# Performance work log

Hardware: AMD Instinct MI355X
Metric: run time of the kernel (lower is better)

Reference implementation:

```python
import jax, jax.numpy as jnp
import numpy as np

BASIS = 30
HIDDEN = 15
MAX_ATOMS = 30
NUM_ATOMS = 110
NUM_GAUSS = 56
T = 3
B = 2048


def setup_inputs() -> dict:
    key = jax.random.key(0)
    ks = jax.random.split(key, 16)
    Z = jax.random.randint(ks[0], (B, MAX_ATOMS), 0, NUM_ATOMS + 1)
    D = jax.random.uniform(ks[1], (B, MAX_ATOMS, MAX_ATOMS, NUM_GAUSS), dtype=jnp.float32)
    sizes = jax.random.randint(ks[2], (B,), 1, MAX_ATOMS + 1)
    s = 0.1
    C_embed = jax.random.normal(ks[3], (NUM_ATOMS + 1, BASIS), dtype=jnp.float32) * s
    df_w = jax.random.normal(ks[4], (NUM_GAUSS, BASIS), dtype=jnp.float32) * s
    df_b = jax.random.normal(ks[5], (BASIS,), dtype=jnp.float32) * s
    cf_w = jax.random.normal(ks[6], (BASIS, BASIS), dtype=jnp.float32) * s
    cf_b = jax.random.normal(ks[7], (BASIS,), dtype=jnp.float32) * s
    fc_w = jax.random.normal(ks[8], (BASIS, BASIS), dtype=jnp.float32) * s  # no bias
    mlp_w1 = jax.random.normal(ks[9], (BASIS, HIDDEN), dtype=jnp.float32) * s
    mlp_b1 = jax.random.normal(ks[10], (HIDDEN,), dtype=jnp.float32) * s
    mlp_w2 = jax.random.normal(ks[11], (HIDDEN, 1), dtype=jnp.float32) * s
    mlp_b2 = jax.random.normal(ks[12], (1,), dtype=jnp.float32) * s
    return {"Z": Z, "D": D, "sizes": sizes, "C_embed": C_embed, "df_w": df_w,
            "df_b": df_b, "cf_w": cf_w, "cf_b": cf_b, "fc_w": fc_w,
            "mlp_w1": mlp_w1, "mlp_b1": mlp_b1, "mlp_w2": mlp_w2, "mlp_b2": mlp_b2}


def reference(Z, D, sizes, C_embed, df_w, df_b, cf_w, cf_b, fc_w,
              mlp_w1, mlp_b1, mlp_w2, mlp_b2):
    # masks from sizes (mask_1d / mask_2d over max_atoms)
    ar = jnp.arange(MAX_ATOMS)
    m1 = (ar[None, :] < sizes[:, None]).astype(D.dtype)            # [B, A]
    m2 = m1[:, :, None] * m1[:, None, :]                           # [B, A, A]

    C = C_embed[Z]                                                 # [B, A, basis]
    d_hat = jnp.einsum('bijg,gk->bijk', D, df_w) + df_b            # [B, A, A, basis]

    for _ in range(T):
        X = C @ cf_w + cf_b                                        # [B, A, basis]
        X = X[:, :, None, :] * d_hat                               # [B, A, A, basis]
        X = jnp.tanh(jnp.einsum('bijh,hk->bijk', X, fc_w))         # [B, A, A, basis]
        C = C + (m2[..., None] * X).sum(axis=1)                    # sum over first atom axis

    E = jnp.tanh(C @ mlp_w1 + mlp_b1) @ mlp_w2 + mlp_b2            # [B, A, 1]
    E = E[..., 0]                                                  # [B, A]
    return (m1 * E).sum(axis=-1)                                   # [B]
```

## Files before the change

kernel.cpp:

```cpp
#include <hip/hip_runtime.h>
#include <hip/hip_bf16.h>

typedef __attribute__((ext_vector_type(8))) short bh8;
typedef __attribute__((ext_vector_type(4))) float f4;

#define MFMA_BF16 __builtin_amdgcn_mfma_f32_16x16x32_bf16

__device__ __forceinline__ unsigned cvtpk(float a, float b) {
  unsigned r;
  asm("v_cvt_pk_bf16_f32 %0, %1, %2" : "=v"(r) : "v"(a), "v"(b));
  return r;
}
__device__ __forceinline__ bh8 mk_bh8(unsigned a, unsigned b, unsigned c, unsigned d) {
  uint4 u;
  u.x = a; u.y = b; u.z = c; u.w = d;
  return __builtin_bit_cast(bh8, u);
}

__device__ __forceinline__ float fast_tanh(float x) {
  float e = __builtin_amdgcn_exp2f(x * 2.885390081777927f);
  return fmaf(-2.f, __builtin_amdgcn_rcpf(e + 1.f), 1.f);
}

__device__ __forceinline__ short bf16hi(float f, float* hf) {
  __hip_bfloat16 h = __float2bfloat16(f);
  *hf = __bfloat162float(h);
  short s;
  __builtin_memcpy(&s, &h, 2);
  return s;
}
__device__ __forceinline__ short bf16s(float f) {
  __hip_bfloat16 h = __float2bfloat16(f);
  short s;
  __builtin_memcpy(&s, &h, 2);
  return s;
}


__global__ __launch_bounds__(256, 4) void mdtnn_phA_mfma(
    const float* __restrict__ Dg, const int* __restrict__ sizesg,
    const float* __restrict__ dfwg, const float* __restrict__ dfbg,
    uint2* __restrict__ dhg)
{
  const int b = blockIdx.x, tid = threadIdx.x;
  const int w = tid >> 6, l = tid & 63;
  const int lr = l & 15, lc = l >> 4;
  const int n = sizesg[b];
  const int nn = n * n;
  const unsigned inv = (65536u + (unsigned)n - 1) / (unsigned)n;

  bh8 Ah[2][2], Al[2][2];
  #pragma unroll
  for (int ht = 0; ht < 2; ++ht) {
    const int h = ht * 16 + lr;
    #pragma unroll
    for (int kc = 0; kc < 2; ++kc) {
      #pragma unroll
      for (int e = 0; e < 8; ++e) {
        const int g = kc * 32 + lc * 8 + e;
        float v = (g < 56 && h < 30) ? dfwg[g * 30 + h] : 0.f;
        float hf;
        Ah[ht][kc][e] = bf16hi(v, &hf);
        Al[ht][kc][e] = bf16s(v - hf);
      }
    }
  }
  float dfbv[2][4];
  #pragma unroll
  for (int ht = 0; ht < 2; ++ht)
    #pragma unroll
    for (int e = 0; e < 4; ++e) {
      const int h = ht * 16 + lc * 4 + e;
      dfbv[ht][e] = (h < 30) ? dfbg[h] : 0.f;
    }

  const float* Db = Dg + (size_t)b * (30 * 30 * 56);
  uint2* dhb = dhg + (size_t)b * (30 * 30 * 8);
  const f4 z4 = {0.f, 0.f, 0.f, 0.f};

  const int tiles = (nn + 15) >> 4;
  for (int t = w; t < tiles; t += 4) {
    const int p_raw = t * 16 + lr;
    const int p = min(p_raw, nn - 1);
    const int i = (int)(((unsigned)p * inv) >> 16);
    const int j = p - i * n;
    const int row = i * 30 + j;
    const float* Dp = Db + (size_t)row * 56;

    float4 q0 = *reinterpret_cast<const float4*>(Dp + lc * 8);
    float4 q1 = *reinterpret_cast<const float4*>(Dp + lc * 8 + 4);
    float4 q2 = {0.f, 0.f, 0.f, 0.f}, q3 = {0.f, 0.f, 0.f, 0.f};
    if (lc < 3) {
      q2 = *reinterpret_cast<const float4*>(Dp + 32 + lc * 8);
      q3 = *reinterpret_cast<const float4*>(Dp + 32 + lc * 8 + 4);
    }
    bh8 B0 = mk_bh8(cvtpk(q0.x, q0.y), cvtpk(q0.z, q0.w),
                    cvtpk(q1.x, q1.y), cvtpk(q1.z, q1.w));
    bh8 B1 = mk_bh8(cvtpk(q2.x, q2.y), cvtpk(q2.z, q2.w),
                    cvtpk(q3.x, q3.y), cvtpk(q3.z, q3.w));

    f4 a0 = z4, a1 = z4;
    a0 = MFMA_BF16(Al[0][0], B0, a0, 0, 0, 0);
    a0 = MFMA_BF16(Ah[0][0], B0, a0, 0, 0, 0);
    a0 = MFMA_BF16(Al[0][1], B1, a0, 0, 0, 0);
    a0 = MFMA_BF16(Ah[0][1], B1, a0, 0, 0, 0);
    a1 = MFMA_BF16(Al[1][0], B0, a1, 0, 0, 0);
    a1 = MFMA_BF16(Ah[1][0], B0, a1, 0, 0, 0);
    a1 = MFMA_BF16(Al[1][1], B1, a1, 0, 0, 0);
    a1 = MFMA_BF16(Ah[1][1], B1, a1, 0, 0, 0);

    if (p_raw < nn) {
      uint2 s0, s1;
      s0.x = cvtpk(a0[0] + dfbv[0][0], a0[1] + dfbv[0][1]);
      s0.y = cvtpk(a0[2] + dfbv[0][2], a0[3] + dfbv[0][3]);
      s1.x = cvtpk(a1[0] + dfbv[1][0], a1[1] + dfbv[1][1]);
      s1.y = cvtpk(a1[2] + dfbv[1][2], a1[3] + dfbv[1][3]);
      dhb[row * 8 + 0 * 4 + lc] = s0;
      dhb[row * 8 + 1 * 4 + lc] = s1;
    }
  }
}

__global__ __launch_bounds__(128, 3) void mdtnn_phB5(
    const int* __restrict__ Zg, const int* __restrict__ sizesg,
    const float* __restrict__ embg, const float* __restrict__ cfwg,
    const float* __restrict__ cfbg, const float* __restrict__ fcwg,
    const float* __restrict__ w1g, const float* __restrict__ b1g,
    const float* __restrict__ w2g, const float* __restrict__ b2g,
    const unsigned* __restrict__ dhg, float* __restrict__ outg)
{
  const int tid = threadIdx.x;
  const int wid = tid >> 6, l = tid & 63;
  const int lr = l & 15, lc = l >> 4;
  const int bm = blockIdx.x;

  __shared__ __align__(16) float buf[2][32][36];
  __shared__ __align__(16) float w1_s[32][16];
  __shared__ float b1_s[16], w2_s[16], wsum[2];

  for (int t = tid; t < 512; t += 128) {
    int k = t >> 4, c = t & 15;
    w1_s[k][c] = (k < 30 && c < 15) ? w1g[k * 15 + c] : 0.f;
  }
  if (tid < 16) {
    b1_s[tid] = (tid < 15) ? b1g[tid] : 0.f;
    w2_s[tid] = (tid < 15) ? w2g[tid] : 0.f;
  }

  const int n = sizesg[bm];
  float (*mybuf)[36] = buf[wid];

  float fcwF0[8], fcwF1[8];
  bh8 cfwB0h, cfwB0l, cfwB1h, cfwB1l;
  #pragma unroll
  for (int e = 0; e < 8; ++e) {
    const int kk = lc * 8 + e;
    const int c1 = lr + 16;
    fcwF0[e] = (kk < 30) ? fcwg[kk * 30 + lr] : 0.f;
    fcwF1[e] = (kk < 30 && c1 < 30) ? fcwg[kk * 30 + c1] : 0.f;
    float g0 = (kk < 30) ? cfwg[kk * 30 + lr] : 0.f;
    float g1 = (kk < 30 && c1 < 30) ? cfwg[kk * 30 + c1] : 0.f;
    float hf;
    cfwB0h[e] = bf16hi(g0, &hf);
    cfwB0l[e] = bf16s(g0 - hf);
    cfwB1h[e] = bf16hi(g1, &hf);
    cfwB1l[e] = bf16s(g1 - hf);
  }
  const float cfb0 = cfbg[lr];
  const float cfb1 = (lr + 16 < 30) ? cfbg[lr + 16] : 0.f;

  f4 C00, C01, C10, C11;
  #pragma unroll
  for (int e = 0; e < 4; ++e) {
    const int r0 = lc * 4 + e;
    const int r1 = 16 + lc * 4 + e;
    const int z0 = Zg[bm * 30 + r0];
    C00[e] = embg[z0 * 30 + lr];
    C01[e] = (lr + 16 < 30) ? embg[z0 * 30 + lr + 16] : 0.f;
    if (r1 < 30) {
      const int z1 = Zg[bm * 30 + r1];
      C10[e] = embg[z1 * 30 + lr];
      C11[e] = (lr + 16 < 30) ? embg[z1 * 30 + lr + 16] : 0.f;
    } else {
      C10[e] = 0.f;
      C11[e] = 0.f;
    }
  }

  const unsigned* dhb = dhg + (size_t)bm * 14400;
  const int n0 = (n + 1) >> 1;
  const int ibeg = wid ? n0 : 0;
  const int iend = wid ? n : n0;
  const f4 z4 = {0.f, 0.f, 0.f, 0.f};

  __syncthreads();

  for (int it = 0; it < 3; ++it) {
    uint4 a0c = {0, 0, 0, 0}, a1c = {0, 0, 0, 0};
    if (ibeg < iend) {
      const unsigned* p = dhb + (size_t)ibeg * 480;
      if (lr < n)      a0c = *reinterpret_cast<const uint4*>(p + lr * 16 + lc * 4);
      if (lr + 16 < n) a1c = *reinterpret_cast<const uint4*>(p + lr * 16 + 256 + lc * 4);
    }

    #pragma unroll
    for (int e = 0; e < 4; ++e) {
      mybuf[lc * 4 + e][lr]           = C00[e];
      mybuf[lc * 4 + e][lr + 16]      = C01[e];
      mybuf[16 + lc * 4 + e][lr]      = C10[e];
      mybuf[16 + lc * 4 + e][lr + 16] = C11[e];
    }
    float cv0[8], cv1[8];
    *reinterpret_cast<float4*>(&cv0[0]) = *reinterpret_cast<const float4*>(&mybuf[lr][lc * 8]);
    *reinterpret_cast<float4*>(&cv0[4]) = *reinterpret_cast<const float4*>(&mybuf[lr][lc * 8 + 4]);
    *reinterpret_cast<float4*>(&cv1[0]) = *reinterpret_cast<const float4*>(&mybuf[16 + lr][lc * 8]);
    *reinterpret_cast<float4*>(&cv1[4]) = *reinterpret_cast<const float4*>(&mybuf[16 + lr][lc * 8 + 4]);

    unsigned h_[4], lo_[4];
    #pragma unroll
    for (int q = 0; q < 4; ++q) {
      unsigned hq = cvtpk(cv0[2 * q], cv0[2 * q + 1]);
      float f0 = __uint_as_float(hq << 16);
      float f1 = __uint_as_float(hq & 0xffff0000u);
      h_[q] = hq;
      lo_[q] = cvtpk(cv0[2 * q] - f0, cv0[2 * q + 1] - f1);
    }
    bh8 Ch0 = mk_bh8(h_[0], h_[1], h_[2], h_[3]);
    bh8 Cl0 = mk_bh8(lo_[0], lo_[1], lo_[2], lo_[3]);
    #pragma unroll
    for (int q = 0; q < 4; ++q) {
      unsigned hq = cvtpk(cv1[2 * q], cv1[2 * q + 1]);
      float f0 = __uint_as_float(hq << 16);
      float f1 = __uint_as_float(hq & 0xffff0000u);
      h_[q] = hq;
      lo_[q] = cvtpk(cv1[2 * q] - f0, cv1[2 * q + 1] - f1);
    }
    bh8 Ch1 = mk_bh8(h_[0], h_[1], h_[2], h_[3]);
    bh8 Cl1 = mk_bh8(lo_[0], lo_[1], lo_[2], lo_[3]);

    f4 d00 = MFMA_BF16(Ch0, cfwB0l, z4, 0, 0, 0);
    d00 = MFMA_BF16(Cl0, cfwB0h, d00, 0, 0, 0);
    d00 = MFMA_BF16(Ch0, cfwB0h, d00, 0, 0, 0);
    f4 d01 = MFMA_BF16(Ch0, cfwB1l, z4, 0, 0, 0);
    d01 = MFMA_BF16(Cl0, cfwB1h, d01, 0, 0, 0);
    d01 = MFMA_BF16(Ch0, cfwB1h, d01, 0, 0, 0);
    f4 d10 = MFMA_BF16(Ch1, cfwB0l, z4, 0, 0, 0);
    d10 = MFMA_BF16(Cl1, cfwB0h, d10, 0, 0, 0);
    d10 = MFMA_BF16(Ch1, cfwB0h, d10, 0, 0, 0);
    f4 d11 = MFMA_BF16(Ch1, cfwB1l, z4, 0, 0, 0);
    d11 = MFMA_BF16(Cl1, cfwB1h, d11, 0, 0, 0);
    d11 = MFMA_BF16(Ch1, cfwB1h, d11, 0, 0, 0);
    #pragma unroll
    for (int e = 0; e < 4; ++e) {
      mybuf[lc * 4 + e][lr]           = d00[e] + cfb0;
      mybuf[lc * 4 + e][lr + 16]      = d01[e] + cfb1;
      mybuf[16 + lc * 4 + e][lr]      = d10[e] + cfb0;
      mybuf[16 + lc * 4 + e][lr + 16] = d11[e] + cfb1;
    }

    f4 i00 = z4, i01 = z4, i10 = z4, i11 = z4;
    for (int i = ibeg; i < iend; ++i) {
      uint4 a0n = {0, 0, 0, 0}, a1n = {0, 0, 0, 0};
      if (i + 1 < iend) {
        const unsigned* p = dhb + (size_t)(i + 1) * 480;
        if (lr < n)      a0n = *reinterpret_cast<const uint4*>(p + lr * 16 + lc * 4);
        if (lr + 16 < n) a1n = *reinterpret_cast<const uint4*>(p + lr * 16 + 256 + lc * 4);
      }
      float4 xA = *reinterpret_cast<const float4*>(&mybuf[i][lc * 8]);
      float4 xB = *reinterpret_cast<const float4*>(&mybuf[i][lc * 8 + 4]);
      float xv[8] = {xA.x, xA.y, xA.z, xA.w, xB.x, xB.y, xB.z, xB.w};
      bh8 W0 = mk_bh8(cvtpk(xv[0] * fcwF0[0], xv[1] * fcwF0[1]),
                      cvtpk(xv[2] * fcwF0[2], xv[3] * fcwF0[3]),
                      cvtpk(xv[4] * fcwF0[4], xv[5] * fcwF0[5]),
                      cvtpk(xv[6] * fcwF0[6], xv[7] * fcwF0[7]));
      bh8 W1 = mk_bh8(cvtpk(xv[0] * fcwF1[0], xv[1] * fcwF1[1]),
                      cvtpk(xv[2] * fcwF1[2], xv[3] * fcwF1[3]),
                      cvtpk(xv[4] * fcwF1[4], xv[5] * fcwF1[5]),
                      cvtpk(xv[6] * fcwF1[6], xv[7] * fcwF1[7]));
      const bh8 A0 = *reinterpret_cast<const bh8*>(&a0c);
      const bh8 A1 = *reinterpret_cast<const bh8*>(&a1c);
      f4 g;
      g = MFMA_BF16(A0, W0, z4, 0, 0, 0);
      #pragma unroll
      for (int e = 0; e < 4; ++e) i00[e] += fast_tanh(g[e]);
      g = MFMA_BF16(A0, W1, z4, 0, 0, 0);
      #pragma unroll
      for (int e = 0; e < 4; ++e) i01[e] += fast_tanh(g[e]);
      g = MFMA_BF16(A1, W0, z4, 0, 0, 0);
      #pragma unroll
      for (int e = 0; e < 4; ++e) i10[e] += fast_tanh(g[e]);
      g = MFMA_BF16(A1, W1, z4, 0, 0, 0);
      #pragma unroll
      for (int e = 0; e < 4; ++e) i11[e] += fast_tanh(g[e]);
      a0c = a0n;
      a1c = a1n;
    }

    #pragma unroll
    for (int e = 0; e < 4; ++e) {
      mybuf[lc * 4 + e][lr]           = i00[e];
      mybuf[lc * 4 + e][lr + 16]      = i01[e];
      mybuf[16 + lc * 4 + e][lr]      = i10[e];
      mybuf[16 + lc * 4 + e][lr + 16] = i11[e];
    }
    __syncthreads();
    #pragma unroll
    for (int e = 0; e < 4; ++e) {
      C00[e] += buf[0][lc * 4 + e][lr];
      C00[e] += buf[1][lc * 4 + e][lr];
      C01[e] += buf[0][lc * 4 + e][lr + 16];
      C01[e] += buf[1][lc * 4 + e][lr + 16];
      C10[e] += buf[0][16 + lc * 4 + e][lr];
      C10[e] += buf[1][16 + lc * 4 + e][lr];
      C11[e] += buf[0][16 + lc * 4 + e][lr + 16];
      C11[e] += buf[1][16 + lc * 4 + e][lr + 16];
    }
    __syncthreads();
  }

  #pragma unroll
  for (int e = 0; e < 4; ++e) {
    mybuf[lc * 4 + e][lr]           = C00[e];
    mybuf[lc * 4 + e][lr + 16]      = C01[e];
    mybuf[16 + lc * 4 + e][lr]      = C10[e];
    mybuf[16 + lc * 4 + e][lr + 16] = C11[e];
  }
  float esum = 0.f;
  for (int t = l + wid * 64; t < n * 16; t += 128) {
    int j = t >> 4, c = t & 15;
    if (c < 15) {
      float a = b1_s[c];
      #pragma unroll
      for (int kc = 0; kc < 8; ++kc) {
        float4 c4 = *reinterpret_cast<const float4*>(&mybuf[j][kc * 4]);
        a = fmaf(c4.x, w1_s[kc * 4 + 0][c], a);
        a = fmaf(c4.y, w1_s[kc * 4 + 1][c], a);
        a = fmaf(c4.z, w1_s[kc * 4 + 2][c], a);
        a = fmaf(c4.w, w1_s[kc * 4 + 3][c], a);
      }
      esum += fast_tanh(a) * w2_s[c];
    }
  }
  #pragma unroll
  for (int off = 32; off; off >>= 1) esum += __shfl_down(esum, off);
  if (l == 0) wsum[wid] = esum;
  __syncthreads();
  if (tid == 0) outg[bm] = wsum[0] + wsum[1] + (float)n * b2g[0];
}

extern "C" void kernel_launch(void* const* d_in, const int* in_sizes, int n_in,
                              void* d_out, int out_size, void* d_ws, size_t ws_size,
                              hipStream_t stream) {
  (void)in_sizes; (void)n_in; (void)ws_size;
  const int*   Z   = (const int*)d_in[0];
  const float* D   = (const float*)d_in[1];
  const int*   sz  = (const int*)d_in[2];
  const float* emb = (const float*)d_in[3];
  const float* dfw = (const float*)d_in[4];
  const float* dfb = (const float*)d_in[5];
  const float* cfw = (const float*)d_in[6];
  const float* cfb = (const float*)d_in[7];
  const float* fcw = (const float*)d_in[8];
  const float* w1  = (const float*)d_in[9];
  const float* b1  = (const float*)d_in[10];
  const float* w2  = (const float*)d_in[11];
  const float* b2  = (const float*)d_in[12];
  float* out = (float*)d_out;
  const int B = out_size;

  mdtnn_phA_mfma<<<dim3(B), dim3(256), 0, stream>>>(D, sz, dfw, dfb, (uint2*)d_ws);
  mdtnn_phB5<<<dim3(B), dim3(128), 0, stream>>>(Z, sz, emb, cfw, cfb, fcw,
                                                w1, b1, w2, b2,
                                                (const unsigned*)d_ws, out);
}
```

Baseline: 108.5 us.

## Use persistent blocks with atomic work-queue scheduling for both phases

Both kernels become persistent: a fixed grid of 1024 blocks pulls molecule indices from a global atomic counter instead of using one block per molecule. Because molecule sizes vary widely, dynamic scheduling is meant to balance load across CUs and amortise per-block weight setup (the fc/cf weight conversion and the MLP weights in shared memory). It adds a memset launch, two atomics and barriers per job, and relies on the workspace having room for the counters after the d_hat buffer.

```diff
diff --git a/kernel.cpp b/kernel.cpp
--- a/kernel.cpp
+++ b/kernel.cpp
@@ -40,14 +40,11 @@
 __global__ __launch_bounds__(256, 4) void mdtnn_phA_mfma(
     const float* __restrict__ Dg, const int* __restrict__ sizesg,
     const float* __restrict__ dfwg, const float* __restrict__ dfbg,
-    uint2* __restrict__ dhg)
+    uint2* __restrict__ dhg, unsigned* __restrict__ ctr, int Bn)
 {
-  const int b = blockIdx.x, tid = threadIdx.x;
+  const int tid = threadIdx.x;
   const int w = tid >> 6, l = tid & 63;
   const int lr = l & 15, lc = l >> 4;
-  const int n = sizesg[b];
-  const int nn = n * n;
-  const unsigned inv = (65536u + (unsigned)n - 1) / (unsigned)n;
 
   bh8 Ah[2][2], Al[2][2];
   #pragma unroll
@@ -73,70 +70,83 @@
       const int h = ht * 16 + lc * 4 + e;
       dfbv[ht][e] = (h < 30) ? dfbg[h] : 0.f;
     }
-
-  const float* Db = Dg + (size_t)b * (30 * 30 * 56);
-  uint2* dhb = dhg + (size_t)b * (30 * 30 * 8);
   const f4 z4 = {0.f, 0.f, 0.f, 0.f};
 
-  const int tiles = (nn + 15) >> 4;
-  for (int t = w; t < tiles; t += 4) {
-    const int p_raw = t * 16 + lr;
-    const int p = min(p_raw, nn - 1);
-    const int i = (int)(((unsigned)p * inv) >> 16);
-    const int j = p - i * n;
-    const int row = i * 30 + j;
-    const float* Dp = Db + (size_t)row * 56;
-
-    float4 q0 = *reinterpret_cast<const float4*>(Dp + lc * 8);
-    float4 q1 = *reinterpret_cast<const float4*>(Dp + lc * 8 + 4);
-    float4 q2 = {0.f, 0.f, 0.f, 0.f}, q3 = {0.f, 0.f, 0.f, 0.f};
-    if (lc < 3) {
-      q2 = *reinterpret_cast<const float4*>(Dp + 32 + lc * 8);
-      q3 = *reinterpret_cast<const float4*>(Dp + 32 + lc * 8 + 4);
-    }
-    bh8 B0 = mk_bh8(cvtpk(q0.x, q0.y), cvtpk(q0.z, q0.w),
-                    cvtpk(q1.x, q1.y), cvtpk(q1.z, q1.w));
-    bh8 B1 = mk_bh8(cvtpk(q2.x, q2.y), cvtpk(q2.z, q2.w),
-                    cvtpk(q3.x, q3.y), cvtpk(q3.z, q3.w));
-
-    f4 a0 = z4, a1 = z4;
-    a0 = MFMA_BF16(Al[0][0], B0, a0, 0, 0, 0);
-    a0 = MFMA_BF16(Ah[0][0], B0, a0, 0, 0, 0);
-    a0 = MFMA_BF16(Al[0][1], B1, a0, 0, 0, 0);
-    a0 = MFMA_BF16(Ah[0][1], B1, a0, 0, 0, 0);
-    a1 = MFMA_BF16(Al[1][0], B0, a1, 0, 0, 0);
-    a1 = MFMA_BF16(Ah[1][0], B0, a1, 0, 0, 0);
-    a1 = MFMA_BF16(Al[1][1], B1, a1, 0, 0, 0);
-    a1 = MFMA_BF16(Ah[1][1], B1, a1, 0, 0, 0);
-
-    if (p_raw < nn) {
-      uint2 s0, s1;
-      s0.x = cvtpk(a0[0] + dfbv[0][0], a0[1] + dfbv[0][1]);
-      s0.y = cvtpk(a0[2] + dfbv[0][2], a0[3] + dfbv[0][3]);
-      s1.x = cvtpk(a1[0] + dfbv[1][0], a1[1] + dfbv[1][1]);
-      s1.y = cvtpk(a1[2] + dfbv[1][2], a1[3] + dfbv[1][3]);
-      dhb[row * 8 + 0 * 4 + lc] = s0;
-      dhb[row * 8 + 1 * 4 + lc] = s1;
-    }
-  }
-}
-
-__global__ __launch_bounds__(128, 3) void mdtnn_phB5(
+  __shared__ int job_s;
+  for (;;) {
+    __syncthreads();
+    if (tid == 0) job_s = (int)atomicAdd(ctr, 1u);
+    __syncthreads();
+    const int b = job_s;
+    if (b >= Bn) break;
+
+    const int n = sizesg[b];
+    const int nn = n * n;
+    const unsigned inv = (65536u + (unsigned)n - 1) / (unsigned)n;
+    const float* Db = Dg + (size_t)b * (30 * 30 * 56);
+    uint2* dhb = dhg + (size_t)b * (30 * 30 * 8);
+
+    const int tiles = (nn + 15) >> 4;
+    for (int t = w; t < tiles; t += 4) {
+      const int p_raw = t * 16 + lr;
+      const int p = min(p_raw, nn - 1);
+      const int i = (int)(((unsigned)p * inv) >> 16);
+      const int j = p - i * n;
+      const int row = i * 30 + j;
+      const float* Dp = Db + (size_t)row * 56;
+
+      float4 q0 = *reinterpret_cast<const float4*>(Dp + lc * 8);
+      float4 q1 = *reinterpret_cast<const float4*>(Dp + lc * 8 + 4);
+      float4 q2 = {0.f, 0.f, 0.f, 0.f}, q3 = {0.f, 0.f, 0.f, 0.f};
+      if (lc < 3) {
+        q2 = *reinterpret_cast<const float4*>(Dp + 32 + lc * 8);
+        q3 = *reinterpret_cast<const float4*>(Dp + 32 + lc * 8 + 4);
+      }
+      bh8 B0 = mk_bh8(cvtpk(q0.x, q0.y), cvtpk(q0.z, q0.w),
+                      cvtpk(q1.x, q1.y), cvtpk(q1.z, q1.w));
+      bh8 B1 = mk_bh8(cvtpk(q2.x, q2.y), cvtpk(q2.z, q2.w),
+                      cvtpk(q3.x, q3.y), cvtpk(q3.z, q3.w));
+
+      f4 a0 = z4, a1 = z4;
+      a0 = MFMA_BF16(Al[0][0], B0, a0, 0, 0, 0);
+      a0 = MFMA_BF16(Ah[0][0], B0, a0, 0, 0, 0);
+      a0 = MFMA_BF16(Al[0][1], B1, a0, 0, 0, 0);
+      a0 = MFMA_BF16(Ah[0][1], B1, a0, 0, 0, 0);
+      a1 = MFMA_BF16(Al[1][0], B0, a1, 0, 0, 0);
+      a1 = MFMA_BF16(Ah[1][0], B0, a1, 0, 0, 0);
+      a1 = MFMA_BF16(Al[1][1], B1, a1, 0, 0, 0);
+      a1 = MFMA_BF16(Ah[1][1], B1, a1, 0, 0, 0);
+
+      if (p_raw < nn) {
+        uint2 s0, s1;
+        s0.x = cvtpk(a0[0] + dfbv[0][0], a0[1] + dfbv[0][1]);
+        s0.y = cvtpk(a0[2] + dfbv[0][2], a0[3] + dfbv[0][3]);
+        s1.x = cvtpk(a1[0] + dfbv[1][0], a1[1] + dfbv[1][1]);
+        s1.y = cvtpk(a1[2] + dfbv[1][2], a1[3] + dfbv[1][3]);
+        dhb[row * 8 + 0 * 4 + lc] = s0;
+        dhb[row * 8 + 1 * 4 + lc] = s1;
+      }
+    }
+  }
+}
+
+__global__ __launch_bounds__(128, 3) void mdtnn_phB7(
     const int* __restrict__ Zg, const int* __restrict__ sizesg,
     const float* __restrict__ embg, const float* __restrict__ cfwg,
     const float* __restrict__ cfbg, const float* __restrict__ fcwg,
     const float* __restrict__ w1g, const float* __restrict__ b1g,
     const float* __restrict__ w2g, const float* __restrict__ b2g,
-    const unsigned* __restrict__ dhg, float* __restrict__ outg)
+    const unsigned* __restrict__ dhg, float* __restrict__ outg,
+    unsigned* __restrict__ ctr, int Bn)
 {
   const int tid = threadIdx.x;
   const int wid = tid >> 6, l = tid & 63;
   const int lr = l & 15, lc = l >> 4;
-  const int bm = blockIdx.x;
 
   __shared__ __align__(16) float buf[2][32][36];
   __shared__ __align__(16) float w1_s[32][16];
   __shared__ float b1_s[16], w2_s[16], wsum[2];
+  __shared__ int job_s;
 
   for (int t = tid; t < 512; t += 128) {
     int k = t >> 4, c = t & 15;
@@ -147,7 +157,6 @@
     w2_s[tid] = (tid < 15) ? w2g[tid] : 0.f;
   }
 
-  const int n = sizesg[bm];
   float (*mybuf)[36] = buf[wid];
 
   float fcwF0[8], fcwF1[8];
@@ -168,39 +177,161 @@
   }
   const float cfb0 = cfbg[lr];
   const float cfb1 = (lr + 16 < 30) ? cfbg[lr + 16] : 0.f;
-
-  f4 C00, C01, C10, C11;
-  #pragma unroll
-  for (int e = 0; e < 4; ++e) {
-    const int r0 = lc * 4 + e;
-    const int r1 = 16 + lc * 4 + e;
-    const int z0 = Zg[bm * 30 + r0];
-    C00[e] = embg[z0 * 30 + lr];
-    C01[e] = (lr + 16 < 30) ? embg[z0 * 30 + lr + 16] : 0.f;
-    if (r1 < 30) {
-      const int z1 = Zg[bm * 30 + r1];
-      C10[e] = embg[z1 * 30 + lr];
-      C11[e] = (lr + 16 < 30) ? embg[z1 * 30 + lr + 16] : 0.f;
-    } else {
-      C10[e] = 0.f;
-      C11[e] = 0.f;
-    }
-  }
-
-  const unsigned* dhb = dhg + (size_t)bm * 14400;
-  const int n0 = (n + 1) >> 1;
-  const int ibeg = wid ? n0 : 0;
-  const int iend = wid ? n : n0;
   const f4 z4 = {0.f, 0.f, 0.f, 0.f};
 
-  __syncthreads();
-
-  for (int it = 0; it < 3; ++it) {
-    uint4 a0c = {0, 0, 0, 0}, a1c = {0, 0, 0, 0};
-    if (ibeg < iend) {
-      const unsigned* p = dhb + (size_t)ibeg * 480;
-      if (lr < n)      a0c = *reinterpret_cast<const uint4*>(p + lr * 16 + lc * 4);
-      if (lr + 16 < n) a1c = *reinterpret_cast<const uint4*>(p + lr * 16 + 256 + lc * 4);
+  for (;;) {
+    __syncthreads();
+    if (tid == 0) job_s = (int)atomicAdd(ctr, 1u);
+    __syncthreads();
+    const int bm = job_s;
+    if (bm >= Bn) break;
+
+    const int n = sizesg[bm];
+    const unsigned* dhb = dhg + (size_t)bm * 14400;
+    const int n0 = (n + 1) >> 1;
+    const int ibeg = wid ? n0 : 0;
+    const int iend = wid ? n : n0;
+    const bool j0ok = (lr < n), j1ok = (lr + 16 < n);
+
+    f4 C00, C01, C10, C11;
+    #pragma unroll
+    for (int e = 0; e < 4; ++e) {
+      const int r0 = lc * 4 + e;
+      const int r1 = 16 + lc * 4 + e;
+      const int z0 = Zg[bm * 30 + r0];
+      C00[e] = embg[z0 * 30 + lr];
+      C01[e] = (lr + 16 < 30) ? embg[z0 * 30 + lr + 16] : 0.f;
+      if (r1 < 30) {
+        const int z1 = Zg[bm * 30 + r1];
+        C10[e] = embg[z1 * 30 + lr];
+        C11[e] = (lr + 16 < 30) ? embg[z1 * 30 + lr + 16] : 0.f;
+      } else {
+        C10[e] = 0.f;
+        C11[e] = 0.f;
+      }
+    }
+
+    for (int it = 0; it < 3; ++it) {
+      uint4 a0c = {0, 0, 0, 0}, a1c = {0, 0, 0, 0};
+      if (ibeg < iend) {
+        const unsigned* p = dhb + (size_t)ibeg * 480;
+        if (j0ok) a0c = *reinterpret_cast<const uint4*>(p + lr * 16 + lc * 4);
+        if (j1ok) a1c = *reinterpret_cast<const uint4*>(p + lr * 16 + 256 + lc * 4);
+      }
+
+      #pragma unroll
+      for (int e = 0; e < 4; ++e) {
+        mybuf[lc * 4 + e][lr]           = C00[e];
+        mybuf[lc * 4 + e][lr + 16]      = C01[e];
+        mybuf[16 + lc * 4 + e][lr]      = C10[e];
+        mybuf[16 + lc * 4 + e][lr + 16] = C11[e];
+      }
+      float cv0[8], cv1[8];
+      *reinterpret_cast<float4*>(&cv0[0]) = *reinterpret_cast<const float4*>(&mybuf[lr][lc * 8]);
+      *reinterpret_cast<float4*>(&cv0[4]) = *reinterpret_cast<const float4*>(&mybuf[lr][lc * 8 + 4]);
+      *reinterpret_cast<float4*>(&cv1[0]) = *reinterpret_cast<const float4*>(&mybuf[16 + lr][lc * 8]);
+      *reinterpret_cast<float4*>(&cv1[4]) = *reinterpret_cast<const float4*>(&mybuf[16 + lr][lc * 8 + 4]);
+
+      unsigned h_[4], lo_[4];
+      #pragma unroll
+      for (int q = 0; q < 4; ++q) {
+        unsigned hq = cvtpk(cv0[2 * q], cv0[2 * q + 1]);
+        float f0 = __uint_as_float(hq << 16);
+        float f1 = __uint_as_float(hq & 0xffff0000u);
+        h_[q] = hq;
+        lo_[q] = cvtpk(cv0[2 * q] - f0, cv0[2 * q + 1] - f1);
+      }
+      bh8 Ch0 = mk_bh8(h_[0], h_[1], h_[2], h_[3]);
+      bh8 Cl0 = mk_bh8(lo_[0], lo_[1], lo_[2], lo_[3]);
+      #pragma unroll
+      for (int q = 0; q < 4; ++q) {
+        unsigned hq = cvtpk(cv1[2 * q], cv1[2 * q + 1]);
+        float f0 = __uint_as_float(hq << 16);
+        float f1 = __uint_as_float(hq & 0xffff0000u);
+        h_[q] = hq;
+        lo_[q] = cvtpk(cv1[2 * q] - f0, cv1[2 * q + 1] - f1);
+      }
+      bh8 Ch1 = mk_bh8(h_[0], h_[1], h_[2], h_[3]);
+      bh8 Cl1 = mk_bh8(lo_[0], lo_[1], lo_[2], lo_[3]);
+
+      f4 d00 = MFMA_BF16(Ch0, cfwB0l, z4, 0, 0, 0);
+      d00 = MFMA_BF16(Cl0, cfwB0h, d00, 0, 0, 0);
+      d00 = MFMA_BF16(Ch0, cfwB0h, d00, 0, 0, 0);
+      f4 d01 = MFMA_BF16(Ch0, cfwB1l, z4, 0, 0, 0);
+      d01 = MFMA_BF16(Cl0, cfwB1h, d01, 0, 0, 0);
+      d01 = MFMA_BF16(Ch0, cfwB1h, d01, 0, 0, 0);
+      f4 d10 = MFMA_BF16(Ch1, cfwB0l, z4, 0, 0, 0);
+      d10 = MFMA_BF16(Cl1, cfwB0h, d10, 0, 0, 0);
+      d10 = MFMA_BF16(Ch1, cfwB0h, d10, 0, 0, 0);
+      f4 d11 = MFMA_BF16(Ch1, cfwB1l, z4, 0, 0, 0);
+      d11 = MFMA_BF16(Cl1, cfwB1h, d11, 0, 0, 0);
+      d11 = MFMA_BF16(Ch1, cfwB1h, d11, 0, 0, 0);
+      #pragma unroll
+      for (int e = 0; e < 4; ++e) {
+        mybuf[lc * 4 + e][lr]           = d00[e] + cfb0;
+        mybuf[lc * 4 + e][lr + 16]      = d01[e] + cfb1;
+        mybuf[16 + lc * 4 + e][lr]      = d10[e] + cfb0;
+        mybuf[16 + lc * 4 + e][lr + 16] = d11[e] + cfb1;
+      }
+
+      f4 i00 = z4, i01 = z4, i10 = z4, i11 = z4;
+      for (int i = ibeg; i < iend; ++i) {
+        uint4 a0n = {0, 0, 0, 0}, a1n = {0, 0, 0, 0};
+        if (i + 1 < iend) {
+          const unsigned* p = dhb + (size_t)(i + 1) * 480;
+          if (j0ok) a0n = *reinterpret_cast<const uint4*>(p + lr * 16 + lc * 4);
+          if (j1ok) a1n = *reinterpret_cast<const uint4*>(p + lr * 16 + 256 + lc * 4);
+        }
+        float4 xA = *reinterpret_cast<const float4*>(&mybuf[i][lc * 8]);
+        float4 xB = *reinterpret_cast<const float4*>(&mybuf[i][lc * 8 + 4]);
+        float xv[8] = {xA.x, xA.y, xA.z, xA.w, xB.x, xB.y, xB.z, xB.w};
+        bh8 W0 = mk_bh8(cvtpk(xv[0] * fcwF0[0], xv[1] * fcwF0[1]),
+                        cvtpk(xv[2] * fcwF0[2], xv[3] * fcwF0[3]),
+                        cvtpk(xv[4] * fcwF0[4], xv[5] * fcwF0[5]),
+                        cvtpk(xv[6] * fcwF0[6], xv[7] * fcwF0[7]));
+        bh8 W1 = mk_bh8(cvtpk(xv[0] * fcwF1[0], xv[1] * fcwF1[1]),
+                        cvtpk(xv[2] * fcwF1[2], xv[3] * fcwF1[3]),
+                        cvtpk(xv[4] * fcwF1[4], xv[5] * fcwF1[5]),
+                        cvtpk(xv[6] * fcwF1[6], xv[7] * fcwF1[7]));
+        const bh8 A0 = __builtin_bit_cast(bh8, a0c);
+        const bh8 A1 = __builtin_bit_cast(bh8, a1c);
+        f4 g;
+        g = MFMA_BF16(A0, W0, z4, 0, 0, 0);
+        #pragma unroll
+        for (int e = 0; e < 4; ++e) i00[e] += fast_tanh(g[e]);
+        g = MFMA_BF16(A0, W1, z4, 0, 0, 0);
+        #pragma unroll
+        for (int e = 0; e < 4; ++e) i01[e] += fast_tanh(g[e]);
+        g = MFMA_BF16(A1, W0, z4, 0, 0, 0);
+        #pragma unroll
+        for (int e = 0; e < 4; ++e) i10[e] += fast_tanh(g[e]);
+        g = MFMA_BF16(A1, W1, z4, 0, 0, 0);
+        #pragma unroll
+        for (int e = 0; e < 4; ++e) i11[e] += fast_tanh(g[e]);
+        a0c = a0n;
+        a1c = a1n;
+      }
+
+      #pragma unroll
+      for (int e = 0; e < 4; ++e) {
+        mybuf[lc * 4 + e][lr]           = i00[e];
+        mybuf[lc * 4 + e][lr + 16]      = i01[e];
+        mybuf[16 + lc * 4 + e][lr]      = i10[e];
+        mybuf[16 + lc * 4 + e][lr + 16] = i11[e];
+      }
+      __syncthreads();
+      #pragma unroll
+      for (int e = 0; e < 4; ++e) {
+        C00[e] += buf[0][lc * 4 + e][lr];
+        C00[e] += buf[1][lc * 4 + e][lr];
+        C01[e] += buf[0][lc * 4 + e][lr + 16];
+        C01[e] += buf[1][lc * 4 + e][lr + 16];
+        C10[e] += buf[0][16 + lc * 4 + e][lr];
+        C10[e] += buf[1][16 + lc * 4 + e][lr];
+        C11[e] += buf[0][16 + lc * 4 + e][lr + 16];
+        C11[e] += buf[1][16 + lc * 4 + e][lr + 16];
+      }
+      __syncthreads();
     }
 
     #pragma unroll
@@ -210,142 +341,28 @@
       mybuf[16 + lc * 4 + e][lr]      = C10[e];
       mybuf[16 + lc * 4 + e][lr + 16] = C11[e];
     }
-    float cv0[8], cv1[8];
-    *reinterpret_cast<float4*>(&cv0[0]) = *reinterpret_cast<const float4*>(&mybuf[lr][lc * 8]);
-    *reinterpret_cast<float4*>(&cv0[4]) = *reinterpret_cast<const float4*>(&mybuf[lr][lc * 8 + 4]);
-    *reinterpret_cast<float4*>(&cv1[0]) = *reinterpret_cast<const float4*>(&mybuf[16 + lr][lc * 8]);
-    *reinterpret_cast<float4*>(&cv1[4]) = *reinterpret_cast<const float4*>(&mybuf[16 + lr][lc * 8 + 4]);
-
-    unsigned h_[4], lo_[4];
-    #pragma unroll
-    for (int q = 0; q < 4; ++q) {
-      unsigned hq = cvtpk(cv0[2 * q], cv0[2 * q + 1]);
-      float f0 = __uint_as_float(hq << 16);
-      float f1 = __uint_as_float(hq & 0xffff0000u);
-      h_[q] = hq;
-      lo_[q] = cvtpk(cv0[2 * q] - f0, cv0[2 * q + 1] - f1);
-    }
-    bh8 Ch0 = mk_bh8(h_[0], h_[1], h_[2], h_[3]);
-    bh8 Cl0 = mk_bh8(lo_[0], lo_[1], lo_[2], lo_[3]);
-    #pragma unroll
-    for (int q = 0; q < 4; ++q) {
-      unsigned hq = cvtpk(cv1[2 * q], cv1[2 * q + 1]);
-      float f0 = __uint_as_float(hq << 16);
-      float f1 = __uint_as_float(hq & 0xffff0000u);
-      h_[q] = hq;
-      lo_[q] = cvtpk(cv1[2 * q] - f0, cv1[2 * q + 1] - f1);
-    }
-    bh8 Ch1 = mk_bh8(h_[0], h_[1], h_[2], h_[3]);
-    bh8 Cl1 = mk_bh8(lo_[0], lo_[1], lo_[2], lo_[3]);
-
-    f4 d00 = MFMA_BF16(Ch0, cfwB0l, z4, 0, 0, 0);
-    d00 = MFMA_BF16(Cl0, cfwB0h, d00, 0, 0, 0);
-    d00 = MFMA_BF16(Ch0, cfwB0h, d00, 0, 0, 0);
-    f4 d01 = MFMA_BF16(Ch0, cfwB1l, z4, 0, 0, 0);
-    d01 = MFMA_BF16(Cl0, cfwB1h, d01, 0, 0, 0);
-    d01 = MFMA_BF16(Ch0, cfwB1h, d01, 0, 0, 0);
-    f4 d10 = MFMA_BF16(Ch1, cfwB0l, z4, 0, 0, 0);
-    d10 = MFMA_BF16(Cl1, cfwB0h, d10, 0, 0, 0);
-    d10 = MFMA_BF16(Ch1, cfwB0h, d10, 0, 0, 0);
-    f4 d11 = MFMA_BF16(Ch1, cfwB1l, z4, 0, 0, 0);
-    d11 = MFMA_BF16(Cl1, cfwB1h, d11, 0, 0, 0);
-    d11 = MFMA_BF16(Ch1, cfwB1h, d11, 0, 0, 0);
-    #pragma unroll
-    for (int e = 0; e < 4; ++e) {
-      mybuf[lc * 4 + e][lr]           = d00[e] + cfb0;
-      mybuf[lc * 4 + e][lr + 16]      = d01[e] + cfb1;
-      mybuf[16 + lc * 4 + e][lr]      = d10[e] + cfb0;
-      mybuf[16 + lc * 4 + e][lr + 16] = d11[e] + cfb1;
-    }
-
-    f4 i00 = z4, i01 = z4, i10 = z4, i11 = z4;
-    for (int i = ibeg; i < iend; ++i) {
-      uint4 a0n = {0, 0, 0, 0}, a1n = {0, 0, 0, 0};
-      if (i + 1 < iend) {
-        const unsigned* p = dhb + (size_t)(i + 1) * 480;
-        if (lr < n)      a0n = *reinterpret_cast<const uint4*>(p + lr * 16 + lc * 4);
-        if (lr + 16 < n) a1n = *reinterpret_cast<const uint4*>(p + lr * 16 + 256 + lc * 4);
-      }
-      float4 xA = *reinterpret_cast<const float4*>(&mybuf[i][lc * 8]);
-      float4 xB = *reinterpret_cast<const float4*>(&mybuf[i][lc * 8 + 4]);
-      float xv[8] = {xA.x, xA.y, xA.z, xA.w, xB.x, xB.y, xB.z, xB.w};
-      bh8 W0 = mk_bh8(cvtpk(xv[0] * fcwF0[0], xv[1] * fcwF0[1]),
-                      cvtpk(xv[2] * fcwF0[2], xv[3] * fcwF0[3]),
-                      cvtpk(xv[4] * fcwF0[4], xv[5] * fcwF0[5]),
-                      cvtpk(xv[6] * fcwF0[6], xv[7] * fcwF0[7]));
-      bh8 W1 = mk_bh8(cvtpk(xv[0] * fcwF1[0], xv[1] * fcwF1[1]),
-                      cvtpk(xv[2] * fcwF1[2], xv[3] * fcwF1[3]),
-                      cvtpk(xv[4] * fcwF1[4], xv[5] * fcwF1[5]),
-                      cvtpk(xv[6] * fcwF1[6], xv[7] * fcwF1[7]));
-      const bh8 A0 = *reinterpret_cast<const bh8*>(&a0c);
-      const bh8 A1 = *reinterpret_cast<const bh8*>(&a1c);
-      f4 g;
-      g = MFMA_BF16(A0, W0, z4, 0, 0, 0);
-      #pragma unroll
-      for (int e = 0; e < 4; ++e) i00[e] += fast_tanh(g[e]);
-      g = MFMA_BF16(A0, W1, z4, 0, 0, 0);
-      #pragma unroll
-      for (int e = 0; e < 4; ++e) i01[e] += fast_tanh(g[e]);
-      g = MFMA_BF16(A1, W0, z4, 0, 0, 0);
-      #pragma unroll
-      for (int e = 0; e < 4; ++e) i10[e] += fast_tanh(g[e]);
-      g = MFMA_BF16(A1, W1, z4, 0, 0, 0);
-      #pragma unroll
-      for (int e = 0; e < 4; ++e) i11[e] += fast_tanh(g[e]);
-      a0c = a0n;
-      a1c = a1n;
-    }
-
-    #pragma unroll
-    for (int e = 0; e < 4; ++e) {
-      mybuf[lc * 4 + e][lr]           = i00[e];
-      mybuf[lc * 4 + e][lr + 16]      = i01[e];
-      mybuf[16 + lc * 4 + e][lr]      = i10[e];
-      mybuf[16 + lc * 4 + e][lr + 16] = i11[e];
-    }
-    __syncthreads();
-    #pragma unroll
-    for (int e = 0; e < 4; ++e) {
-      C00[e] += buf[0][lc * 4 + e][lr];
-      C00[e] += buf[1][lc * 4 + e][lr];
-      C01[e] += buf[0][lc * 4 + e][lr + 16];
-      C01[e] += buf[1][lc * 4 + e][lr + 16];
-      C10[e] += buf[0][16 + lc * 4 + e][lr];
-      C10[e] += buf[1][16 + lc * 4 + e][lr];
-      C11[e] += buf[0][16 + lc * 4 + e][lr + 16];
-      C11[e] += buf[1][16 + lc * 4 + e][lr + 16];
-    }
-    __syncthreads();
-  }
-
-  #pragma unroll
-  for (int e = 0; e < 4; ++e) {
-    mybuf[lc * 4 + e][lr]           = C00[e];
-    mybuf[lc * 4 + e][lr + 16]      = C01[e];
-    mybuf[16 + lc * 4 + e][lr]      = C10[e];
-    mybuf[16 + lc * 4 + e][lr + 16] = C11[e];
-  }
-  float esum = 0.f;
-  for (int t = l + wid * 64; t < n * 16; t += 128) {
-    int j = t >> 4, c = t & 15;
-    if (c < 15) {
-      float a = b1_s[c];
-      #pragma unroll
-      for (int kc = 0; kc < 8; ++kc) {
-        float4 c4 = *reinterpret_cast<const float4*>(&mybuf[j][kc * 4]);
-        a = fmaf(c4.x, w1_s[kc * 4 + 0][c], a);
-        a = fmaf(c4.y, w1_s[kc * 4 + 1][c], a);
-        a = fmaf(c4.z, w1_s[kc * 4 + 2][c], a);
-        a = fmaf(c4.w, w1_s[kc * 4 + 3][c], a);
-      }
-      esum += fast_tanh(a) * w2_s[c];
-    }
-  }
-  #pragma unroll
-  for (int off = 32; off; off >>= 1) esum += __shfl_down(esum, off);
-  if (l == 0) wsum[wid] = esum;
-  __syncthreads();
-  if (tid == 0) outg[bm] = wsum[0] + wsum[1] + (float)n * b2g[0];
+    float esum = 0.f;
+    for (int t = l + wid * 64; t < n * 16; t += 128) {
+      int j = t >> 4, c = t & 15;
+      if (c < 15) {
+        float a = b1_s[c];
+        #pragma unroll
+        for (int kc = 0; kc < 8; ++kc) {
+          float4 c4 = *reinterpret_cast<const float4*>(&mybuf[j][kc * 4]);
+          a = fmaf(c4.x, w1_s[kc * 4 + 0][c], a);
+          a = fmaf(c4.y, w1_s[kc * 4 + 1][c], a);
+          a = fmaf(c4.z, w1_s[kc * 4 + 2][c], a);
+          a = fmaf(c4.w, w1_s[kc * 4 + 3][c], a);
+        }
+        esum += fast_tanh(a) * w2_s[c];
+      }
+    }
+    #pragma unroll
+    for (int off = 32; off; off >>= 1) esum += __shfl_down(esum, off);
+    if (l == 0) wsum[wid] = esum;
+    __syncthreads();
+    if (tid == 0) outg[bm] = wsum[0] + wsum[1] + (float)n * b2g[0];
+  }
 }
 
 extern "C" void kernel_launch(void* const* d_in, const int* in_sizes, int n_in,
@@ -368,8 +385,14 @@
   float* out = (float*)d_out;
   const int B = out_size;
 
-  mdtnn_phA_mfma<<<dim3(B), dim3(256), 0, stream>>>(D, sz, dfw, dfb, (uint2*)d_ws);
-  mdtnn_phB5<<<dim3(B), dim3(128), 0, stream>>>(Z, sz, emb, cfw, cfb, fcw,
-                                                w1, b1, w2, b2,
-                                                (const unsigned*)d_ws, out);
-}
+  const size_t DHB = (size_t)B * 30 * 30 * 64;
+  unsigned* ctrs = (unsigned*)((char*)d_ws + DHB);
+  hipMemsetAsync(ctrs, 0, 2 * sizeof(unsigned), stream);
+
+  mdtnn_phA_mfma<<<dim3(1024), dim3(256), 0, stream>>>(D, sz, dfw, dfb,
+                                                       (uint2*)d_ws, ctrs + 0, B);
+  mdtnn_phB7<<<dim3(1024), dim3(128), 0, stream>>>(Z, sz, emb, cfw, cfb, fcw,
+                                                   w1, b1, w2, b2,
+                                                   (const unsigned*)d_ws, out,
+                                                   ctrs + 1, B);
+}
```

After: 132.4 us. +22.1%, slower.
